# Kernel tuning notes

Hardware: AMD Instinct MI355X
Metric: run time of the kernel (lower is better)

The kernel has to match this reference:

```python
import jax, jax.numpy as jnp
import numpy as np

B, S, D, H = 1, 4096, 1024, 16
HD = D // H  # head_dim = 64
NEG = -1e9

def setup_inputs() -> dict:
    key = jax.random.key(0)
    ks = jax.random.split(key, 5)
    scale = 1.0 / np.sqrt(D)
    x = jax.random.normal(ks[0], (B, S, D), dtype=jnp.float32)
    Wq = jax.random.normal(ks[1], (D, D), dtype=jnp.float32) * scale
    Wk = jax.random.normal(ks[2], (D, D), dtype=jnp.float32) * scale
    Wv = jax.random.normal(ks[3], (D, D), dtype=jnp.float32) * scale
    Wo = jax.random.normal(ks[4], (D, D), dtype=jnp.float32) * scale
    mask = jnp.tril(jnp.ones((S, S), dtype=bool))[None, None]  # [1,1,S,S] causal
    return {"x": x, "mask": mask, "Wq": Wq, "Wk": Wk, "Wv": Wv, "Wo": Wo}

def reference(x, mask, Wq, Wk, Wv, Wo):
    # Linear projections (bias=False). nn.Linear computes x @ W.T; weights here
    # are stored as [out, in] so we use x @ W.T for faithfulness.
    q = x @ Wq.T  # [B,S,D]
    k = x @ Wk.T
    v = x @ Wv.T
    def split_heads(t):
        return t.reshape(B, S, H, HD).transpose(0, 2, 1, 3)  # [B,H,S,HD]
    q, k, v = split_heads(q), split_heads(k), split_heads(v)
    scores = jnp.einsum("bhqd,bhkd->bhqk", q, k) / jnp.sqrt(jnp.float32(HD))
    scores = jnp.where(mask, scores, NEG)
    attn = jax.nn.softmax(scores, axis=-1)  # dropout p=0.0 -> identity
    out = jnp.einsum("bhqk,bhkd->bhqd", attn, v)  # [B,H,S,HD]
    out = out.transpose(0, 2, 1, 3).reshape(B, S, D)
    return out @ Wo.T
```

## Files before the change

### kernel.cpp

```cpp
#include <hip/hip_runtime.h>
#include <hip/hip_bf16.h>


typedef __bf16 bf16x8 __attribute__((ext_vector_type(8)));
typedef __bf16 bf16x4 __attribute__((ext_vector_type(4)));
typedef float f32x4 __attribute__((ext_vector_type(4)));

#define GAS __attribute__((address_space(1)))
#define LAS __attribute__((address_space(3)))

__device__ __forceinline__ void async_copy16(const void* g, void* l) {
  __builtin_amdgcn_global_load_lds((const GAS unsigned int*)g,
                                   (LAS unsigned int*)l, 16, 0, 0);
}

__global__ __launch_bounds__(256) void cvt_all(const float* __restrict__ x,
                                               const float* __restrict__ Wq,
                                               const float* __restrict__ Wk,
                                               const float* __restrict__ Wv,
                                               const float* __restrict__ Wo,
                                               __bf16* __restrict__ xb,
                                               __bf16* __restrict__ Wc,
                                               __bf16* __restrict__ Wob) {
  int b = blockIdx.x;
  const float* src;
  __bf16* dst;
  if (b < 4096)      { src = x  + (b       ) * 1024; dst = xb  + (long)b * 1024; }
  else if (b < 5120) { src = Wq + (b - 4096) * 1024; dst = Wc  + (long)(b - 4096) * 1024; }
  else if (b < 6144) { src = Wk + (b - 5120) * 1024; dst = Wc  + (1l << 20) + (long)(b - 5120) * 1024; }
  else if (b < 7168) { src = Wv + (b - 6144) * 1024; dst = Wc  + (2l << 20) + (long)(b - 6144) * 1024; }
  else               { src = Wo + (b - 7168) * 1024; dst = Wob + (long)(b - 7168) * 1024; }
  int i = threadIdx.x * 4;
  float4 f = *(const float4*)(src + i);
  bf16x4 o;
  o[0] = (__bf16)f.x; o[1] = (__bf16)f.y; o[2] = (__bf16)f.z; o[3] = (__bf16)f.w;
  *(bf16x4*)(dst + i) = o;
}

__global__ __launch_bounds__(256) void gemm_qkv(const __bf16* __restrict__ A,
                                                const __bf16* __restrict__ B,
                                                __bf16* __restrict__ Qb,
                                                __bf16* __restrict__ Kf,
                                                __bf16* __restrict__ Vf) {
  const int K = 1024;
  __shared__ __bf16 As[128 * 32];
  __shared__ __bf16 Bs[128 * 32];
  const int tid = threadIdx.x;
  const int lane = tid & 63, wv = tid >> 6;
  const int l15 = lane & 15, quad = lane >> 4;
  const int wm = wv >> 1, wn = wv & 1;
  const int mbase = blockIdx.y * 128, nbase = blockIdx.x * 128;
  const bool kswap = (nbase >= 1024) && (nbase < 2048);

  f32x4 acc[4][4] = {};

  for (int k0 = 0; k0 < K; k0 += 32) {
    __syncthreads();
#pragma unroll
    for (int q = 0; q < 2; ++q) {
      int i = q * 256 + tid;
      int row = i >> 2, kg = i & 3;
      const __bf16* ga = A + (long)(mbase + row) * K + k0 + kg * 8;
      const __bf16* gb = B + (long)(nbase + row) * K + k0 + kg * 8;
      char* la = (char*)As + (q * 256 + wv * 64) * 16;
      char* lb = (char*)Bs + (q * 256 + wv * 64) * 16;
      async_copy16(ga, la);
      async_copy16(gb, lb);
    }
    __syncthreads();
    bf16x8 af[4], bfr[4];
#pragma unroll
    for (int i = 0; i < 4; ++i)
      af[i] = *(const bf16x8*)&As[(wm * 64 + i * 16 + l15) * 32 + quad * 8];
#pragma unroll
    for (int j = 0; j < 4; ++j)
      bfr[j] = *(const bf16x8*)&Bs[(wn * 64 + j * 16 + l15) * 32 + quad * 8];
    if (kswap) {
#pragma unroll
      for (int i = 0; i < 4; ++i)
#pragma unroll
        for (int j = 0; j < 4; ++j)
          acc[i][j] = __builtin_amdgcn_mfma_f32_16x16x32_bf16(bfr[j], af[i], acc[i][j], 0, 0, 0);
    } else {
#pragma unroll
      for (int i = 0; i < 4; ++i)
#pragma unroll
        for (int j = 0; j < 4; ++j)
          acc[i][j] = __builtin_amdgcn_mfma_f32_16x16x32_bf16(af[i], bfr[j], acc[i][j], 0, 0, 0);
    }
  }

  if (nbase < 1024) {
    const float QS = 0.18033688011112043f;
#pragma unroll
    for (int i = 0; i < 4; ++i)
#pragma unroll
      for (int j = 0; j < 4; ++j) {
        int col = nbase + wn * 64 + j * 16 + l15;
#pragma unroll
        for (int r = 0; r < 4; ++r) {
          int row = mbase + wm * 64 + i * 16 + quad * 4 + r;
          Qb[(long)row * 1024 + col] = (__bf16)(acc[i][j][r] * QS);
        }
      }
  } else if (nbase < 2048) {
#pragma unroll
    for (int i = 0; i < 4; ++i)
#pragma unroll
      for (int j = 0; j < 4; ++j) {
        int d0 = nbase - 1024 + wn * 64 + j * 16 + quad * 4;
        int h = d0 >> 6, dd = d0 & 63;
        int kk = dd >> 5, qf = (dd >> 3) & 3, e0 = dd & 7;
        int kt = mbase + wm * 64 + i * 16 + l15;
        int tile = kt >> 6;
        long off = ((long)(h * 64 + tile) * 8 + i * 2 + kk) * 512 + (qf * 16 + l15) * 8 + e0;
        union { __bf16 b[4]; uint2 u; } pk;
#pragma unroll
        for (int r = 0; r < 4; ++r) pk.b[r] = (__bf16)acc[i][j][r];
        *(uint2*)(Kf + off) = pk.u;
      }
  } else {
#pragma unroll
    for (int i = 0; i < 4; ++i)
#pragma unroll
      for (int j = 0; j < 4; ++j) {
        int col = nbase - 2048 + wn * 64 + j * 16 + l15;
        int h = col >> 6, dd = col & 63;
        int jd = dd >> 4, lv = dd & 15;
        int kt0 = mbase + wm * 64 + i * 16 + quad * 4;
        int tile = kt0 >> 6, w6 = kt0 & 63;
        int t = w6 >> 5, qv = (w6 >> 3) & 3, e0 = w6 & 7;
        long off = ((long)(h * 64 + tile) * 8 + jd * 2 + t) * 512 + (qv * 16 + lv) * 8 + e0;
        union { __bf16 b[4]; uint2 u; } pk;
#pragma unroll
        for (int r = 0; r < 4; ++r) pk.b[r] = (__bf16)acc[i][j][r];
        *(uint2*)(Vf + off) = pk.u;
      }
  }
}

__global__ __launch_bounds__(256) void gemm_wo(const __bf16* __restrict__ A,
                                               const __bf16* __restrict__ B,
                                               float* __restrict__ C) {
  const int K = 1024, N = 1024;
  __shared__ __bf16 As[128 * 32];
  __shared__ __bf16 Bs[64 * 32];
  const int tid = threadIdx.x;
  const int lane = tid & 63, wv = tid >> 6;
  const int l15 = lane & 15, quad = lane >> 4;
  const int wm = wv >> 1, wn = wv & 1;
  const int mbase = blockIdx.y * 128, nbase = blockIdx.x * 64;

  f32x4 acc[4][2] = {};

  for (int k0 = 0; k0 < K; k0 += 32) {
    __syncthreads();
#pragma unroll
    for (int q = 0; q < 2; ++q) {
      int i = q * 256 + tid;
      int row = i >> 2, kg = i & 3;
      const __bf16* ga = A + (long)(mbase + row) * K + k0 + kg * 8;
      char* la = (char*)As + (q * 256 + wv * 64) * 16;
      async_copy16(ga, la);
    }
    {
      int row = tid >> 2, kg = tid & 3;
      const __bf16* gb = B + (long)(nbase + row) * K + k0 + kg * 8;
      char* lb = (char*)Bs + (wv * 64) * 16;
      async_copy16(gb, lb);
    }
    __syncthreads();
    bf16x8 af[4], bfr[2];
#pragma unroll
    for (int i = 0; i < 4; ++i)
      af[i] = *(const bf16x8*)&As[(wm * 64 + i * 16 + l15) * 32 + quad * 8];
#pragma unroll
    for (int j = 0; j < 2; ++j)
      bfr[j] = *(const bf16x8*)&Bs[(wn * 32 + j * 16 + l15) * 32 + quad * 8];
#pragma unroll
    for (int i = 0; i < 4; ++i)
#pragma unroll
      for (int j = 0; j < 2; ++j)
        acc[i][j] = __builtin_amdgcn_mfma_f32_16x16x32_bf16(af[i], bfr[j], acc[i][j], 0, 0, 0);
  }
#pragma unroll
  for (int i = 0; i < 4; ++i)
#pragma unroll
    for (int j = 0; j < 2; ++j)
#pragma unroll
      for (int r = 0; r < 4; ++r) {
        int row = mbase + wm * 64 + i * 16 + quad * 4 + r;
        int col = nbase + wn * 32 + j * 16 + l15;
        C[(long)row * N + col] = acc[i][j][r];
      }
}

__global__ __launch_bounds__(512, 2) void flash_attn(const __bf16* __restrict__ Qb,
                                                     const __bf16* __restrict__ Kf,
                                                     const __bf16* __restrict__ Vf,
                                                     __bf16* __restrict__ AO) {
  __shared__ float Ms[3][64][76];
  const int tid = threadIdx.x;
  const int lane = tid & 63, l15 = lane & 15, quad = lane >> 4;
  const int w = tid >> 6;
  const int s = w >> 2, qtr = w & 3;
  const int b = blockIdx.x;
  const int h = (b & 7) + 8 * ((b >> 3) & 1);
  const int rest = b >> 4;
  const int P = rest * 2 + s;
  const int hoff = h * 64;

  const __bf16* Kh = Kf + (long)h * 64 * 4096;
  const __bf16* Vh = Vf + (long)h * 64 * 4096;

  for (int pass = 0; pass < 2; ++pass) {
    const int T = pass ? (63 - P) : P;
    bf16x8 qf[4][2];
#pragma unroll
    for (int g = 0; g < 4; ++g) {
      const int qrow = T * 64 + g * 16 + l15;
      qf[g][0] = *(const bf16x8*)(Qb + (long)qrow * 1024 + hoff + quad * 8);
      qf[g][1] = *(const bf16x8*)(Qb + (long)qrow * 1024 + hoff + 32 + quad * 8);
    }

    const int nkt = T + 1;
    const int kt0 = (nkt * qtr) >> 2;
    const int kt1 = (nkt * (qtr + 1)) >> 2;
    f32x4 o_acc[4][4] = {};
    float l_acc[4] = {0.0f, 0.0f, 0.0f, 0.0f};

    bf16x8 kc[8];
    if (kt0 < kt1) {
      const __bf16* Kt = Kh + (long)kt0 * 4096;
#pragma unroll
      for (int f = 0; f < 8; ++f)
        kc[f] = *(const bf16x8*)(Kt + f * 512 + lane * 8);
    }

    for (int kt = kt0; kt < kt1; ++kt) {
      const __bf16* Vt = Vh + (long)kt * 4096;

      bf16x8 va[8];
#pragma unroll
      for (int f = 0; f < 8; ++f)
        va[f] = *(const bf16x8*)(Vt + f * 512 + lane * 8);

      unsigned dj[4][4][2];
#pragma unroll
      for (int g = 0; g < 4; ++g) {
        f32x4 stg[4] = {};
#pragma unroll
        for (int j = 0; j < 4; ++j) {
          stg[j] = __builtin_amdgcn_mfma_f32_16x16x32_bf16(kc[j * 2 + 0], qf[g][0], stg[j], 0, 0, 0);
          stg[j] = __builtin_amdgcn_mfma_f32_16x16x32_bf16(kc[j * 2 + 1], qf[g][1], stg[j], 0, 0, 0);
        }

        if (kt == nkt - 1) {
          const int dq = g * 16 + l15;
#pragma unroll
          for (int j = 0; j < 4; ++j)
#pragma unroll
            for (int r = 0; r < 4; ++r)
              if (j * 16 + quad * 4 + r > dq) stg[j][r] = -3.0e38f;
        }

        float ps = 0.0f;
#pragma unroll
        for (int j = 0; j < 4; ++j) {
          f32x4 pj;
#pragma unroll
          for (int r = 0; r < 4; ++r) pj[r] = __builtin_amdgcn_exp2f(stg[j][r]);
          ps += (pj[0] + pj[1]) + (pj[2] + pj[3]);
          union { __bf16 h2[2]; unsigned u; } p0, p1;
          p0.h2[0] = (__bf16)pj[0]; p0.h2[1] = (__bf16)pj[1];
          p1.h2[0] = (__bf16)pj[2]; p1.h2[1] = (__bf16)pj[3];
          dj[g][j][0] = p0.u;
          dj[g][j][1] = p1.u;
        }
        l_acc[g] += ps;
      }

      if (kt + 1 < kt1) {
        const __bf16* Kt = Kh + (long)(kt + 1) * 4096;
#pragma unroll
        for (int f = 0; f < 8; ++f)
          kc[f] = *(const bf16x8*)(Kt + f * 512 + lane * 8);
      }

#pragma unroll
      for (int g = 0; g < 4; ++g)
#pragma unroll
        for (int t = 0; t < 2; ++t) {
          unsigned m0 = dj[g][2 * t + 0][0], m2 = dj[g][2 * t + 1][0];
          unsigned m1 = dj[g][2 * t + 0][1], m3 = dj[g][2 * t + 1][1];
          asm volatile("v_permlane32_swap_b32 %0, %1" : "+v"(m0), "+v"(m2));
          asm volatile("v_permlane32_swap_b32 %0, %1" : "+v"(m1), "+v"(m3));
          asm volatile("v_permlane16_swap_b32 %0, %1" : "+v"(m0), "+v"(m2));
          asm volatile("v_permlane16_swap_b32 %0, %1" : "+v"(m1), "+v"(m3));
          union { unsigned u[4]; bf16x8 v; } Bf;
          Bf.u[0] = m0; Bf.u[1] = m1; Bf.u[2] = m2; Bf.u[3] = m3;
#pragma unroll
          for (int jd = 0; jd < 4; ++jd)
            o_acc[g][jd] = __builtin_amdgcn_mfma_f32_16x16x32_bf16(va[jd * 2 + t], Bf.v, o_acc[g][jd], 0, 0, 0);
        }
    }

    for (int ms = 0; ms < 2; ++ms) {
      if (s == ms && qtr) {
#pragma unroll
        for (int g = 0; g < 4; ++g)
#pragma unroll
          for (int jd = 0; jd < 4; ++jd)
            *(f32x4*)&Ms[qtr - 1][lane][g * 16 + jd * 4] = o_acc[g][jd];
        f32x4 lv;
#pragma unroll
        for (int g = 0; g < 4; ++g) lv[g] = l_acc[g];
        *(f32x4*)&Ms[qtr - 1][lane][64] = lv;
      }
      __syncthreads();
      if (s == ms && !qtr) {
#pragma unroll
        for (int g = 0; g < 4; ++g) {
          float la = l_acc[g];
#pragma unroll
          for (int u = 0; u < 3; ++u) {
#pragma unroll
            for (int jd = 0; jd < 4; ++jd)
              o_acc[g][jd] += *(const f32x4*)&Ms[u][lane][g * 16 + jd * 4];
            la += Ms[u][lane][64 + g];
          }
          la += __shfl_xor(la, 16);
          la += __shfl_xor(la, 32);
          const float inv = 1.0f / la;
          const int qrow = T * 64 + g * 16 + l15;
#pragma unroll
          for (int jd = 0; jd < 4; ++jd) {
            bf16x4 ob;
#pragma unroll
            for (int r = 0; r < 4; ++r) ob[r] = (__bf16)(o_acc[g][jd][r] * inv);
            *(bf16x4*)(AO + (long)qrow * 1024 + hoff + jd * 16 + quad * 4) = ob;
          }
        }
      }
      __syncthreads();
    }
  }
}

extern "C" void kernel_launch(void* const* d_in, const int* in_sizes, int n_in,
                              void* d_out, int out_size, void* d_ws, size_t ws_size,
                              hipStream_t stream) {
  const float* x  = (const float*)d_in[0];
  const float* Wq = (const float*)d_in[2];
  const float* Wk = (const float*)d_in[3];
  const float* Wv = (const float*)d_in[4];
  const float* Wo = (const float*)d_in[5];
  float* out = (float*)d_out;

  char* ws = (char*)d_ws;
  __bf16* xb  = (__bf16*)ws;
  __bf16* Wc  = (__bf16*)(ws + (8u << 20));
  __bf16* Wob = (__bf16*)(ws + (14u << 20));
  __bf16* Qb  = (__bf16*)(ws + (16u << 20));
  __bf16* Kfr = (__bf16*)(ws + (24u << 20));
  __bf16* Vfr = (__bf16*)(ws + (32u << 20));
  __bf16* AO  = (__bf16*)(ws + (40u << 20));

  cvt_all<<<8192, 256, 0, stream>>>(x, Wq, Wk, Wv, Wo, xb, Wc, Wob);

  dim3 g1(3072 / 128, 4096 / 128);
  gemm_qkv<<<g1, 256, 0, stream>>>(xb, Wc, Qb, Kfr, Vfr);

  flash_attn<<<256, 512, 0, stream>>>(Qb, Kfr, Vfr, AO);

  dim3 g2(1024 / 64, 4096 / 128);
  gemm_wo<<<g2, 256, 0, stream>>>(AO, Wob, out);
}
```

Before: 239.6 us.

## Split flash attention into per-tile blocks with two-way KV split

The attention kernel now launches 1024 blocks of 256 threads instead of 256 blocks of 512 threads. Each block owns one 64-row query tile: four waves each take 32 query rows and one half of the key range, and the two halves are merged through a smaller shared buffer with a single barrier. Tiles are ordered largest-first instead of pairing a short and a long tile in two passes. V loads are split into two halves and issued around the softmax to cut register pressure. The intent is better load balance and occupancy, at the cost of reloading K/V per 32-row group and doing less MFMA work per K/V fragment.

```diff
diff --git a/kernel.cpp b/kernel.cpp
--- a/kernel.cpp
+++ b/kernel.cpp
@@ -195,154 +195,164 @@
       }
 }
 
-__global__ __launch_bounds__(512, 2) void flash_attn(const __bf16* __restrict__ Qb,
+__global__ __launch_bounds__(256, 2) void flash_attn(const __bf16* __restrict__ Qb,
                                                      const __bf16* __restrict__ Kf,
                                                      const __bf16* __restrict__ Vf,
                                                      __bf16* __restrict__ AO) {
-  __shared__ float Ms[3][64][76];
+  __shared__ float Ms[2][64][36];
   const int tid = threadIdx.x;
   const int lane = tid & 63, l15 = lane & 15, quad = lane >> 4;
   const int w = tid >> 6;
-  const int s = w >> 2, qtr = w & 3;
+  const int u = w >> 1, hf = w & 1;
   const int b = blockIdx.x;
   const int h = (b & 7) + 8 * ((b >> 3) & 1);
-  const int rest = b >> 4;
-  const int P = rest * 2 + s;
+  const int T = 63 - (b >> 4);
   const int hoff = h * 64;
 
   const __bf16* Kh = Kf + (long)h * 64 * 4096;
   const __bf16* Vh = Vf + (long)h * 64 * 4096;
 
-  for (int pass = 0; pass < 2; ++pass) {
-    const int T = pass ? (63 - P) : P;
-    bf16x8 qf[4][2];
-#pragma unroll
-    for (int g = 0; g < 4; ++g) {
-      const int qrow = T * 64 + g * 16 + l15;
-      qf[g][0] = *(const bf16x8*)(Qb + (long)qrow * 1024 + hoff + quad * 8);
-      qf[g][1] = *(const bf16x8*)(Qb + (long)qrow * 1024 + hoff + 32 + quad * 8);
-    }
-
-    const int nkt = T + 1;
-    const int kt0 = (nkt * qtr) >> 2;
-    const int kt1 = (nkt * (qtr + 1)) >> 2;
-    f32x4 o_acc[4][4] = {};
-    float l_acc[4] = {0.0f, 0.0f, 0.0f, 0.0f};
-
-    bf16x8 kc[8];
-    if (kt0 < kt1) {
-      const __bf16* Kt = Kh + (long)kt0 * 4096;
+  bf16x8 qf[2][2];
+#pragma unroll
+  for (int g = 0; g < 2; ++g) {
+    const int qrow = T * 64 + u * 32 + g * 16 + l15;
+    qf[g][0] = *(const bf16x8*)(Qb + (long)qrow * 1024 + hoff + quad * 8);
+    qf[g][1] = *(const bf16x8*)(Qb + (long)qrow * 1024 + hoff + 32 + quad * 8);
+  }
+
+  const int nkt = T + 1;
+  const int kt0 = hf ? (nkt >> 1) : 0;
+  const int kt1 = hf ? nkt : (nkt >> 1);
+  f32x4 o_acc[2][4] = {};
+  float l_acc[2] = {0.0f, 0.0f};
+
+  bf16x8 kc[8];
+  if (kt0 < kt1) {
+    const __bf16* Kt = Kh + (long)kt0 * 4096;
+#pragma unroll
+    for (int f = 0; f < 8; ++f)
+      kc[f] = *(const bf16x8*)(Kt + f * 512 + lane * 8);
+  }
+
+  for (int kt = kt0; kt < kt1; ++kt) {
+    const __bf16* Vt = Vh + (long)kt * 4096;
+
+    f32x4 stg[2][4] = {};
+#pragma unroll
+    for (int g = 0; g < 2; ++g)
+#pragma unroll
+      for (int j = 0; j < 4; ++j) {
+        stg[g][j] = __builtin_amdgcn_mfma_f32_16x16x32_bf16(kc[j * 2 + 0], qf[g][0], stg[g][j], 0, 0, 0);
+        stg[g][j] = __builtin_amdgcn_mfma_f32_16x16x32_bf16(kc[j * 2 + 1], qf[g][1], stg[g][j], 0, 0, 0);
+      }
+
+    bf16x8 va0[4];
+#pragma unroll
+    for (int jd = 0; jd < 4; ++jd)
+      va0[jd] = *(const bf16x8*)(Vt + (jd * 2) * 512 + lane * 8);
+
+    if (kt + 1 < kt1) {
+      const __bf16* Kt = Kh + (long)(kt + 1) * 4096;
 #pragma unroll
       for (int f = 0; f < 8; ++f)
         kc[f] = *(const bf16x8*)(Kt + f * 512 + lane * 8);
     }
 
-    for (int kt = kt0; kt < kt1; ++kt) {
-      const __bf16* Vt = Vh + (long)kt * 4096;
-
-      bf16x8 va[8];
-#pragma unroll
-      for (int f = 0; f < 8; ++f)
-        va[f] = *(const bf16x8*)(Vt + f * 512 + lane * 8);
-
-      unsigned dj[4][4][2];
-#pragma unroll
-      for (int g = 0; g < 4; ++g) {
-        f32x4 stg[4] = {};
-#pragma unroll
-        for (int j = 0; j < 4; ++j) {
-          stg[j] = __builtin_amdgcn_mfma_f32_16x16x32_bf16(kc[j * 2 + 0], qf[g][0], stg[j], 0, 0, 0);
-          stg[j] = __builtin_amdgcn_mfma_f32_16x16x32_bf16(kc[j * 2 + 1], qf[g][1], stg[j], 0, 0, 0);
-        }
-
-        if (kt == nkt - 1) {
-          const int dq = g * 16 + l15;
-#pragma unroll
-          for (int j = 0; j < 4; ++j)
-#pragma unroll
-            for (int r = 0; r < 4; ++r)
-              if (j * 16 + quad * 4 + r > dq) stg[j][r] = -3.0e38f;
-        }
-
-        float ps = 0.0f;
-#pragma unroll
-        for (int j = 0; j < 4; ++j) {
-          f32x4 pj;
-#pragma unroll
-          for (int r = 0; r < 4; ++r) pj[r] = __builtin_amdgcn_exp2f(stg[j][r]);
-          ps += (pj[0] + pj[1]) + (pj[2] + pj[3]);
-          union { __bf16 h2[2]; unsigned u; } p0, p1;
-          p0.h2[0] = (__bf16)pj[0]; p0.h2[1] = (__bf16)pj[1];
-          p1.h2[0] = (__bf16)pj[2]; p1.h2[1] = (__bf16)pj[3];
-          dj[g][j][0] = p0.u;
-          dj[g][j][1] = p1.u;
-        }
-        l_acc[g] += ps;
-      }
-
-      if (kt + 1 < kt1) {
-        const __bf16* Kt = Kh + (long)(kt + 1) * 4096;
-#pragma unroll
-        for (int f = 0; f < 8; ++f)
-          kc[f] = *(const bf16x8*)(Kt + f * 512 + lane * 8);
-      }
-
-#pragma unroll
-      for (int g = 0; g < 4; ++g)
-#pragma unroll
-        for (int t = 0; t < 2; ++t) {
-          unsigned m0 = dj[g][2 * t + 0][0], m2 = dj[g][2 * t + 1][0];
-          unsigned m1 = dj[g][2 * t + 0][1], m3 = dj[g][2 * t + 1][1];
-          asm volatile("v_permlane32_swap_b32 %0, %1" : "+v"(m0), "+v"(m2));
-          asm volatile("v_permlane32_swap_b32 %0, %1" : "+v"(m1), "+v"(m3));
-          asm volatile("v_permlane16_swap_b32 %0, %1" : "+v"(m0), "+v"(m2));
-          asm volatile("v_permlane16_swap_b32 %0, %1" : "+v"(m1), "+v"(m3));
-          union { unsigned u[4]; bf16x8 v; } Bf;
-          Bf.u[0] = m0; Bf.u[1] = m1; Bf.u[2] = m2; Bf.u[3] = m3;
-#pragma unroll
-          for (int jd = 0; jd < 4; ++jd)
-            o_acc[g][jd] = __builtin_amdgcn_mfma_f32_16x16x32_bf16(va[jd * 2 + t], Bf.v, o_acc[g][jd], 0, 0, 0);
-        }
-    }
-
-    for (int ms = 0; ms < 2; ++ms) {
-      if (s == ms && qtr) {
-#pragma unroll
-        for (int g = 0; g < 4; ++g)
-#pragma unroll
-          for (int jd = 0; jd < 4; ++jd)
-            *(f32x4*)&Ms[qtr - 1][lane][g * 16 + jd * 4] = o_acc[g][jd];
-        f32x4 lv;
-#pragma unroll
-        for (int g = 0; g < 4; ++g) lv[g] = l_acc[g];
-        *(f32x4*)&Ms[qtr - 1][lane][64] = lv;
-      }
-      __syncthreads();
-      if (s == ms && !qtr) {
-#pragma unroll
-        for (int g = 0; g < 4; ++g) {
-          float la = l_acc[g];
-#pragma unroll
-          for (int u = 0; u < 3; ++u) {
-#pragma unroll
-            for (int jd = 0; jd < 4; ++jd)
-              o_acc[g][jd] += *(const f32x4*)&Ms[u][lane][g * 16 + jd * 4];
-            la += Ms[u][lane][64 + g];
-          }
-          la += __shfl_xor(la, 16);
-          la += __shfl_xor(la, 32);
-          const float inv = 1.0f / la;
-          const int qrow = T * 64 + g * 16 + l15;
-#pragma unroll
-          for (int jd = 0; jd < 4; ++jd) {
-            bf16x4 ob;
-#pragma unroll
-            for (int r = 0; r < 4; ++r) ob[r] = (__bf16)(o_acc[g][jd][r] * inv);
-            *(bf16x4*)(AO + (long)qrow * 1024 + hoff + jd * 16 + quad * 4) = ob;
-          }
-        }
-      }
-      __syncthreads();
+    if (kt == nkt - 1) {
+#pragma unroll
+      for (int g = 0; g < 2; ++g) {
+        const int dq = u * 32 + g * 16 + l15;
+#pragma unroll
+        for (int j = 0; j < 4; ++j)
+#pragma unroll
+          for (int r = 0; r < 4; ++r)
+            if (j * 16 + quad * 4 + r > dq) stg[g][j][r] = -3.0e38f;
+      }
+    }
+
+    unsigned dj[2][4][2];
+#pragma unroll
+    for (int g = 0; g < 2; ++g) {
+      float ps = 0.0f;
+#pragma unroll
+      for (int j = 0; j < 4; ++j) {
+        f32x4 pj;
+#pragma unroll
+        for (int r = 0; r < 4; ++r) pj[r] = __builtin_amdgcn_exp2f(stg[g][j][r]);
+        ps += (pj[0] + pj[1]) + (pj[2] + pj[3]);
+        union { __bf16 h2[2]; unsigned uu; } p0, p1;
+        p0.h2[0] = (__bf16)pj[0]; p0.h2[1] = (__bf16)pj[1];
+        p1.h2[0] = (__bf16)pj[2]; p1.h2[1] = (__bf16)pj[3];
+        dj[g][j][0] = p0.uu;
+        dj[g][j][1] = p1.uu;
+      }
+      l_acc[g] += ps;
+    }
+
+    bf16x8 va1[4];
+#pragma unroll
+    for (int jd = 0; jd < 4; ++jd)
+      va1[jd] = *(const bf16x8*)(Vt + (jd * 2 + 1) * 512 + lane * 8);
+
+#pragma unroll
+    for (int g = 0; g < 2; ++g) {
+      unsigned m0 = dj[g][0][0], m2 = dj[g][1][0];
+      unsigned m1 = dj[g][0][1], m3 = dj[g][1][1];
+      asm volatile("v_permlane32_swap_b32 %0, %1" : "+v"(m0), "+v"(m2));
+      asm volatile("v_permlane32_swap_b32 %0, %1" : "+v"(m1), "+v"(m3));
+      asm volatile("v_permlane16_swap_b32 %0, %1" : "+v"(m0), "+v"(m2));
+      asm volatile("v_permlane16_swap_b32 %0, %1" : "+v"(m1), "+v"(m3));
+      union { unsigned u4[4]; bf16x8 v; } Bf;
+      Bf.u4[0] = m0; Bf.u4[1] = m1; Bf.u4[2] = m2; Bf.u4[3] = m3;
+#pragma unroll
+      for (int jd = 0; jd < 4; ++jd)
+        o_acc[g][jd] = __builtin_amdgcn_mfma_f32_16x16x32_bf16(va0[jd], Bf.v, o_acc[g][jd], 0, 0, 0);
+    }
+#pragma unroll
+    for (int g = 0; g < 2; ++g) {
+      unsigned m0 = dj[g][2][0], m2 = dj[g][3][0];
+      unsigned m1 = dj[g][2][1], m3 = dj[g][3][1];
+      asm volatile("v_permlane32_swap_b32 %0, %1" : "+v"(m0), "+v"(m2));
+      asm volatile("v_permlane32_swap_b32 %0, %1" : "+v"(m1), "+v"(m3));
+      asm volatile("v_permlane16_swap_b32 %0, %1" : "+v"(m0), "+v"(m2));
+      asm volatile("v_permlane16_swap_b32 %0, %1" : "+v"(m1), "+v"(m3));
+      union { unsigned u4[4]; bf16x8 v; } Bf;
+      Bf.u4[0] = m0; Bf.u4[1] = m1; Bf.u4[2] = m2; Bf.u4[3] = m3;
+#pragma unroll
+      for (int jd = 0; jd < 4; ++jd)
+        o_acc[g][jd] = __builtin_amdgcn_mfma_f32_16x16x32_bf16(va1[jd], Bf.v, o_acc[g][jd], 0, 0, 0);
+    }
+  }
+
+  if (hf) {
+#pragma unroll
+    for (int g = 0; g < 2; ++g)
+#pragma unroll
+      for (int jd = 0; jd < 4; ++jd)
+        *(f32x4*)&Ms[u][lane][g * 16 + jd * 4] = o_acc[g][jd];
+    Ms[u][lane][32] = l_acc[0];
+    Ms[u][lane][33] = l_acc[1];
+  }
+  __syncthreads();
+  if (!hf) {
+#pragma unroll
+    for (int g = 0; g < 2; ++g) {
+      float la = l_acc[g];
+#pragma unroll
+      for (int jd = 0; jd < 4; ++jd)
+        o_acc[g][jd] += *(const f32x4*)&Ms[u][lane][g * 16 + jd * 4];
+      la += Ms[u][lane][32 + g];
+      la += __shfl_xor(la, 16);
+      la += __shfl_xor(la, 32);
+      const float inv = 1.0f / la;
+      const int qrow = T * 64 + u * 32 + g * 16 + l15;
+#pragma unroll
+      for (int jd = 0; jd < 4; ++jd) {
+        bf16x4 ob;
+#pragma unroll
+        for (int r = 0; r < 4; ++r) ob[r] = (__bf16)(o_acc[g][jd][r] * inv);
+        *(bf16x4*)(AO + (long)qrow * 1024 + hoff + jd * 16 + quad * 4) = ob;
+      }
     }
   }
 }
@@ -371,7 +381,7 @@
   dim3 g1(3072 / 128, 4096 / 128);
   gemm_qkv<<<g1, 256, 0, stream>>>(xb, Wc, Qb, Kfr, Vfr);
 
-  flash_attn<<<256, 512, 0, stream>>>(Qb, Kfr, Vfr, AO);
+  flash_attn<<<1024, 256, 0, stream>>>(Qb, Kfr, Vfr, AO);
 
   dim3 g2(1024 / 64, 4096 / 128);
   gemm_wo<<<g2, 256, 0, stream>>>(AO, Wob, out);
```

Result: faster. 233.8 us (-2.4%).
